# Kernel optimization log

Measured on AMD Instinct MI355X. Metric: run time of the kernel, lower is better.

The kernel has to match this reference:

```python
import jax, jax.numpy as jnp
import numpy as np

MAX_SEQ = 2048
NUM_HEADS = 32
NUM_KV_HEADS = 4
HEAD_DIM = 256
HIDDEN = 4096
ROTARY_DIM = 64  # head_dim * partial_rotary_factor(0.25)
THETA = 10000000.0
EPS = 1e-6
GROUPS = NUM_HEADS // NUM_KV_HEADS
SCALE = 1.0 / np.sqrt(HEAD_DIM)


def rms_norm(x, w):
    xf = x.astype(jnp.float32)
    norm = jax.lax.rsqrt(jnp.mean(xf * xf, axis=-1, keepdims=True) + EPS)
    return (xf * norm * w).astype(x.dtype)


def partial_rope(x, position):
    # x: [B, H, 1, D]; rotate first ROTARY_DIM dims (split-half convention)
    half = ROTARY_DIM // 2
    inv_freq = 1.0 / (THETA ** (jnp.arange(half, dtype=jnp.float32) / half))
    freqs = position.astype(jnp.float32) * inv_freq  # [half]
    cos = jnp.cos(freqs).reshape(1, 1, 1, -1)
    sin = jnp.sin(freqs).reshape(1, 1, 1, -1)
    x1 = x[..., :half]
    x2 = x[..., half:ROTARY_DIM]
    x_pass = x[..., ROTARY_DIM:]
    rot = jnp.concatenate([x1 * cos - x2 * sin, x2 * cos + x1 * sin], axis=-1)
    return jnp.concatenate([rot, x_pass], axis=-1)


def setup_inputs() -> dict:
    key = jax.random.key(0)
    ks = jax.random.split(key, 10)
    pos = 1500
    position = jnp.array([pos], dtype=jnp.int32)
    idx = jnp.arange(MAX_SEQ)
    mask = jnp.where(idx <= pos, 0.0, -1e9).astype(jnp.float32).reshape(1, 1, 1, MAX_SEQ)
    onehot = (idx == pos).astype(jnp.float32).reshape(1, 1, MAX_SEQ, 1)
    return {
        "x": jax.random.normal(ks[0], (1, 1, HIDDEN), dtype=jnp.float32),
        "position": position,
        "mask": mask,
        "k_cache": jax.random.normal(ks[1], (1, NUM_KV_HEADS, MAX_SEQ, HEAD_DIM), dtype=jnp.float32),
        "v_cache": jax.random.normal(ks[2], (1, NUM_KV_HEADS, MAX_SEQ, HEAD_DIM), dtype=jnp.float32),
        "onehot": onehot,
        "q_proj_w": jax.random.normal(ks[3], (2 * NUM_HEADS * HEAD_DIM, HIDDEN), dtype=jnp.float32) * 0.02,
        "k_proj_w": jax.random.normal(ks[4], (NUM_KV_HEADS * HEAD_DIM, HIDDEN), dtype=jnp.float32) * 0.02,
        "v_proj_w": jax.random.normal(ks[5], (NUM_KV_HEADS * HEAD_DIM, HIDDEN), dtype=jnp.float32) * 0.02,
        "o_proj_w": jax.random.normal(ks[6], (HIDDEN, NUM_HEADS * HEAD_DIM), dtype=jnp.float32) * 0.02,
        "q_norm_w": jnp.ones((HEAD_DIM,), dtype=jnp.float32),
        "k_norm_w": jnp.ones((HEAD_DIM,), dtype=jnp.float32),
    }


def reference(x, position, mask, k_cache, v_cache, onehot,
              q_proj_w, k_proj_w, v_proj_w, o_proj_w, q_norm_w, k_norm_w):
    B, T, _ = x.shape  # B=T=1
    # Q + gate interleaved per head
    qg = jnp.einsum('bth,oh->bto', x, q_proj_w).reshape(B, T, NUM_HEADS, 2 * HEAD_DIM)
    q = qg[..., :HEAD_DIM]                      # [B,T,H,D]
    gate = qg[..., HEAD_DIM:].reshape(B, T, -1)  # [B,T,H*D]
    q = jnp.transpose(q, (0, 2, 1, 3))           # [B,H,T,D]
    k = jnp.einsum('bth,oh->bto', x, k_proj_w).reshape(B, T, NUM_KV_HEADS, HEAD_DIM).transpose(0, 2, 1, 3)
    v = jnp.einsum('bth,oh->bto', x, v_proj_w).reshape(B, T, NUM_KV_HEADS, HEAD_DIM).transpose(0, 2, 1, 3)
    q = rms_norm(q, q_norm_w)
    k = rms_norm(k, k_norm_w)
    q = partial_rope(q, position)
    k = partial_rope(k, position)
    # full-buffer onehot cache update (same math as mul_/add_)
    k_cache = k_cache * (1.0 - onehot) + k * onehot  # [B,KV,S,D]
    v_cache = v_cache * (1.0 - onehot) + v * onehot
    # GQA: group query heads over kv heads without materializing expanded KV
    qg_heads = q.reshape(B, NUM_KV_HEADS, GROUPS, T, HEAD_DIM)
    attn = jnp.einsum('bgktd,bgsd->bgkts', qg_heads, k_cache) * SCALE  # [B,KV,G,T,S]
    attn = attn + mask[:, :, None]  # mask [B,1,1,T,S] broadcast
    attn = jax.nn.softmax(attn, axis=-1)
    out = jnp.einsum('bgkts,bgsd->bgktd', attn, v_cache)  # [B,KV,G,T,D]
    out = out.reshape(B, NUM_HEADS, T, HEAD_DIM).transpose(0, 2, 1, 3).reshape(B, T, -1)
    out = out * jax.nn.sigmoid(gate)
    return jnp.einsum('bto,ho->bth', out, o_proj_w)
```

## Files before the change

### kernel.cpp

```cpp
#include <hip/hip_runtime.h>
#include <math.h>

#define MAX_SEQ   2048
#define NUM_HEADS 32
#define NUM_KV    4
#define HEAD_DIM  256
#define HIDDEN    4096
#define ROT_DIM   64
#define GROUPS    8
#define SCALE     0.0625f
#define CHUNK     32
#define NCHUNK    (MAX_SEQ / CHUNK)

typedef float f4 __attribute__((ext_vector_type(4)));

__device__ inline f4 ntload4(const float* p) {
    return __builtin_nontemporal_load(reinterpret_cast<const f4*>(p));
}

__global__ void rope_table(const int* __restrict__ posp, float* __restrict__ tab) {
    const int i = threadIdx.x;
    if (i < 32) {
        const double inv_freq = pow(10000000.0, -(double)i / 32.0);
        const double ang = (double)posp[0] * inv_freq;
        tab[i]      = (float)cos(ang);
        tab[i + 32] = (float)sin(ang);
    }
}

__global__ __launch_bounds__(256) void gemv_qkv(
    const float* __restrict__ x,
    const float* __restrict__ qw,
    const float* __restrict__ kw,
    const float* __restrict__ vw,
    float* __restrict__ out)
{
    const int wave = threadIdx.x >> 6;
    const int lane = threadIdx.x & 63;
    const int row  = blockIdx.x * 4 + wave;

    const float* w;
    if (row < 16384)      w = qw + (size_t)row * HIDDEN;
    else if (row < 17408) w = kw + (size_t)(row - 16384) * HIDDEN;
    else                  w = vw + (size_t)(row - 17408) * HIDDEN;

    float acc = 0.f;
#pragma unroll
    for (int it = 0; it < HIDDEN / 256; ++it) {
        const int idx = it * 256 + lane * 4;
        f4 wv = ntload4(w + idx);
        f4 xv = *reinterpret_cast<const f4*>(x + idx);
        acc += wv[0] * xv[0] + wv[1] * xv[1] + wv[2] * xv[2] + wv[3] * xv[3];
    }
#pragma unroll
    for (int off = 32; off >= 1; off >>= 1) acc += __shfl_xor(acc, off);
    if (lane == 0) out[row] = acc;
}

__global__ __launch_bounds__(256) void attn_partial(
    const float* __restrict__ qkv,
    const float* __restrict__ qnw,
    const float* __restrict__ knw,
    const float* __restrict__ kcache,
    const float* __restrict__ vcache,
    const float* __restrict__ tab,
    const int*   __restrict__ posp,
    float* __restrict__ part_m,
    float* __restrict__ part_l,
    float* __restrict__ part_acc)
{
    const int kv  = blockIdx.x;
    const int c   = blockIdx.y;
    const int pos = posp[0];
    const int s0  = c * CHUNK;
    const int tid = threadIdx.x;

    if (s0 > pos) {
        if (tid == 0) {
#pragma unroll
            for (int g = 0; g < GROUPS; ++g) {
                const int pid = (kv * GROUPS + g) * NCHUNK + c;
                part_m[pid] = -1e30f; part_l[pid] = 0.f;
            }
        }
        return;
    }
    const int s1 = min(s0 + CHUNK, pos + 1);

    const int lane = tid & 63;
    const int wave = tid >> 6;
    const int d    = tid;

    float vals[9];
#pragma unroll
    for (int g = 0; g < GROUPS; ++g)
        vals[g] = qkv[(kv * GROUPS + g) * 512 + d];
    vals[8] = qkv[16384 + kv * HEAD_DIM + d];

    __shared__ float ssred[9][4];
    {
        float sq[9];
#pragma unroll
        for (int g = 0; g < 9; ++g) sq[g] = vals[g] * vals[g];
#pragma unroll
        for (int off = 32; off >= 1; off >>= 1) {
#pragma unroll
            for (int g = 0; g < 9; ++g) sq[g] += __shfl_xor(sq[g], off);
        }
        if (lane == 0) {
#pragma unroll
            for (int g = 0; g < 9; ++g) ssred[g][wave] = sq[g];
        }
    }
    __syncthreads();

    __shared__ __align__(16) float qn[9][HEAD_DIM];
    {
        const float qw_ = qnw[d];
        const float kw_ = knw[d];
#pragma unroll
        for (int g = 0; g < 9; ++g) {
            const float tot  = ssred[g][0] + ssred[g][1] + ssred[g][2] + ssred[g][3];
            const float norm = rsqrtf(tot * (1.0f / HEAD_DIM) + 1e-6f);
            qn[g][d] = vals[g] * norm * (g < 8 ? qw_ : kw_);
        }
    }
    __syncthreads();

    {
        const bool rot = (d < ROT_DIM);
        const int  i   = d & 31;
        const float co = tab[i];
        const float si = tab[i + 32];
        float rv[9];
#pragma unroll
        for (int g = 0; g < 9; ++g) {
            const float x1 = qn[g][i];
            const float x2 = qn[g][i + 32];
            rv[g] = (d < 32) ? (x1 * co - x2 * si) : (x2 * co + x1 * si);
        }
        __syncthreads();
        if (rot) {
#pragma unroll
            for (int g = 0; g < 9; ++g) qn[g][d] = rv[g];
        }
        __syncthreads();
    }

    const float* kbase = kcache + (size_t)kv * MAX_SEQ * HEAD_DIM;
    const float* vbase = vcache + (size_t)kv * MAX_SEQ * HEAD_DIM;

    f4 q8[GROUPS];
#pragma unroll
    for (int g = 0; g < GROUPS; ++g)
        q8[g] = *reinterpret_cast<const f4*>(&qn[g][lane * 4]);

    __shared__ float sc[GROUPS][CHUNK];
    __shared__ __align__(16) float pl[GROUPS][CHUNK];
    __shared__ float mh[GROUPS], lh[GROUPS];

    {
        const int i0 = wave * 8;
        f4 kvec[8];
#pragma unroll
        for (int j = 0; j < 8; ++j) {
            const int s = s0 + i0 + j;
            if (s < pos) kvec[j] = ntload4(kbase + (size_t)s * HEAD_DIM + lane * 4);
            else         kvec[j] = *reinterpret_cast<const f4*>(&qn[8][lane * 4]);
        }
#pragma unroll
        for (int j = 0; j < 8; ++j) {
            const int s = s0 + i0 + j;
            const bool valid = (s < s1);
            float part[GROUPS];
#pragma unroll
            for (int g = 0; g < GROUPS; ++g) {
                f4 t = q8[g] * kvec[j];
                part[g] = t[0] + t[1] + t[2] + t[3];
            }
#pragma unroll
            for (int off = 32; off >= 1; off >>= 1) {
#pragma unroll
                for (int g = 0; g < GROUPS; ++g)
                    part[g] += __shfl_xor(part[g], off);
            }
            if (lane == 0) {
#pragma unroll
                for (int g = 0; g < GROUPS; ++g)
                    sc[g][i0 + j] = valid ? part[g] * SCALE : -1e30f;
            }
        }
    }
    __syncthreads();

    {
        const int h = tid >> 5;
        const int j = tid & 31;
        float v = sc[h][j];
        float m = v;
#pragma unroll
        for (int off = 16; off >= 1; off >>= 1)
            m = fmaxf(m, __shfl_xor(m, off));
        const float p = expf(v - m);
        pl[h][j] = p;
        float ls = p;
#pragma unroll
        for (int off = 16; off >= 1; off >>= 1)
            ls += __shfl_xor(ls, off);
        if (j == 0) { mh[h] = m; lh[h] = ls; }
    }
    __syncthreads();

    float acc[GROUPS];
#pragma unroll
    for (int g = 0; g < GROUPS; ++g) acc[g] = 0.f;
    const float* vnew = qkv + 17408 + kv * HEAD_DIM;
#pragma unroll
    for (int i4 = 0; i4 < CHUNK / 4; ++i4) {
        float vv[4];
#pragma unroll
        for (int u = 0; u < 4; ++u) {
            const int s = s0 + i4 * 4 + u;
            vv[u] = (s < pos) ? __builtin_nontemporal_load(vbase + (size_t)s * HEAD_DIM + d)
                              : vnew[d];
        }
        f4 p4[GROUPS];
#pragma unroll
        for (int g = 0; g < GROUPS; ++g)
            p4[g] = *reinterpret_cast<const f4*>(&pl[g][i4 * 4]);
#pragma unroll
        for (int u = 0; u < 4; ++u) {
#pragma unroll
            for (int g = 0; g < GROUPS; ++g)
                acc[g] += p4[g][u] * vv[u];
        }
    }
#pragma unroll
    for (int g = 0; g < GROUPS; ++g) {
        const int pid = (kv * GROUPS + g) * NCHUNK + c;
        part_acc[(size_t)pid * HEAD_DIM + d] = acc[g];
        if (tid == 0) { part_m[pid] = mh[g]; part_l[pid] = lh[g]; }
    }
}

__global__ __launch_bounds__(256) void attn_combine(
    const float* __restrict__ part_m,
    const float* __restrict__ part_l,
    const float* __restrict__ part_acc,
    const float* __restrict__ qkv,
    float* __restrict__ attn_gated)
{
    const int h = blockIdx.x;
    const int d = threadIdx.x;

    float M = -1e30f;
    for (int c = 0; c < NCHUNK; ++c) M = fmaxf(M, part_m[h * NCHUNK + c]);

    float L = 0.f, acc = 0.f;
    for (int c = 0; c < NCHUNK; ++c) {
        const float lc = part_l[h * NCHUNK + c];
        if (lc > 0.f) {
            const float w = expf(part_m[h * NCHUNK + c] - M);
            L   += lc * w;
            acc += part_acc[(size_t)(h * NCHUNK + c) * HEAD_DIM + d] * w;
        }
    }
    const float o   = acc / L;
    const float g   = qkv[h * 512 + 256 + d];
    const float sig = 1.0f / (1.0f + expf(-g));
    attn_gated[h * HEAD_DIM + d] = o * sig;
}

__global__ __launch_bounds__(256) void gemv_o(
    const float* __restrict__ vec,
    const float* __restrict__ w,
    float* __restrict__ out)
{
    const int wave = threadIdx.x >> 6;
    const int lane = threadIdx.x & 63;
    const int row  = blockIdx.x * 4 + wave;
    const float* wr = w + (size_t)row * 8192;

    float acc = 0.f;
#pragma unroll
    for (int it = 0; it < 8192 / 256; ++it) {
        const int idx = it * 256 + lane * 4;
        f4 wv = ntload4(wr + idx);
        f4 xv = *reinterpret_cast<const f4*>(vec + idx);
        acc += wv[0] * xv[0] + wv[1] * xv[1] + wv[2] * xv[2] + wv[3] * xv[3];
    }
#pragma unroll
    for (int off = 32; off >= 1; off >>= 1) acc += __shfl_xor(acc, off);
    if (lane == 0) out[row] = acc;
}

extern "C" void kernel_launch(void* const* d_in, const int* in_sizes, int n_in,
                              void* d_out, int out_size, void* d_ws, size_t ws_size,
                              hipStream_t stream) {
    const float* x        = (const float*)d_in[0];
    const int*   position = (const int*)  d_in[1];
    const float* k_cache  = (const float*)d_in[3];
    const float* v_cache  = (const float*)d_in[4];
    const float* q_proj_w = (const float*)d_in[6];
    const float* k_proj_w = (const float*)d_in[7];
    const float* v_proj_w = (const float*)d_in[8];
    const float* o_proj_w = (const float*)d_in[9];
    const float* q_norm_w = (const float*)d_in[10];
    const float* k_norm_w = (const float*)d_in[11];
    float* out = (float*)d_out;

    float* ws         = (float*)d_ws;
    float* qkv        = ws;
    float* tab        = ws + 18432;
    float* part_m     = ws + 18496;
    float* part_l     = ws + 20544;
    float* part_acc   = ws + 22592;
    float* attn_gated = ws + 546880;

    rope_table<<<1, 64, 0, stream>>>(position, tab);
    gemv_qkv<<<18432 / 4, 256, 0, stream>>>(x, q_proj_w, k_proj_w, v_proj_w, qkv);
    dim3 g2(NUM_KV, NCHUNK);
    attn_partial<<<g2, 256, 0, stream>>>(qkv, q_norm_w, k_norm_w,
                                         k_cache, v_cache, tab, position,
                                         part_m, part_l, part_acc);
    attn_combine<<<NUM_HEADS, 256, 0, stream>>>(part_m, part_l, part_acc, qkv,
                                                attn_gated);
    gemv_o<<<4096 / 4, 256, 0, stream>>>(attn_gated, o_proj_w, out);
}
```

Before: 108.0 us.

## Fold rope table into QKV GEMV, two rows per wave, prefetch KV earlier, smaller chunks

The separate rope_table launch is folded into an extra block of the QKV GEMV. Both GEMVs now compute two output rows per wave and set launch_bounds occupancy hints. Attention partials use 16-position chunks, doubling the number of blocks, and issue the K and V cache loads before the RMS-norm and RoPE stage so their latency overlaps that work. The cost is more partial results for attn_combine to merge, higher register pressure from the prefetched values, and a reshuffled workspace layout.

```diff
diff --git a/kernel.cpp b/kernel.cpp
--- a/kernel.cpp
+++ b/kernel.cpp
@@ -9,7 +9,7 @@
 #define ROT_DIM   64
 #define GROUPS    8
 #define SCALE     0.0625f
-#define CHUNK     32
+#define CHUNK     16
 #define NCHUNK    (MAX_SEQ / CHUNK)
 
 typedef float f4 __attribute__((ext_vector_type(4)));
@@ -18,43 +18,54 @@
     return __builtin_nontemporal_load(reinterpret_cast<const f4*>(p));
 }
 
-__global__ void rope_table(const int* __restrict__ posp, float* __restrict__ tab) {
-    const int i = threadIdx.x;
-    if (i < 32) {
-        const double inv_freq = pow(10000000.0, -(double)i / 32.0);
-        const double ang = (double)posp[0] * inv_freq;
-        tab[i]      = (float)cos(ang);
-        tab[i + 32] = (float)sin(ang);
-    }
-}
-
-__global__ __launch_bounds__(256) void gemv_qkv(
+__global__ __launch_bounds__(256, 4) void gemv_qkv(
     const float* __restrict__ x,
     const float* __restrict__ qw,
     const float* __restrict__ kw,
     const float* __restrict__ vw,
-    float* __restrict__ out)
+    const int*   __restrict__ posp,
+    float* __restrict__ out,
+    float* __restrict__ tab)
 {
+    if (blockIdx.x == 2304) {
+        const int i = threadIdx.x;
+        if (i < 32) {
+            const double inv_freq = pow(10000000.0, -(double)i / 32.0);
+            const double ang = (double)posp[0] * inv_freq;
+            tab[i]      = (float)cos(ang);
+            tab[i + 32] = (float)sin(ang);
+        }
+        return;
+    }
     const int wave = threadIdx.x >> 6;
     const int lane = threadIdx.x & 63;
-    const int row  = blockIdx.x * 4 + wave;
-
-    const float* w;
-    if (row < 16384)      w = qw + (size_t)row * HIDDEN;
-    else if (row < 17408) w = kw + (size_t)(row - 16384) * HIDDEN;
-    else                  w = vw + (size_t)(row - 17408) * HIDDEN;
-
-    float acc = 0.f;
+    const int wid  = blockIdx.x * 4 + wave;
+    const int r0   = wid * 2;
+    const int r1   = r0 + 1;
+
+    const float* w0 = (r0 < 16384) ? qw + (size_t)r0 * HIDDEN
+                    : (r0 < 17408) ? kw + (size_t)(r0 - 16384) * HIDDEN
+                                   : vw + (size_t)(r0 - 17408) * HIDDEN;
+    const float* w1 = (r1 < 16384) ? qw + (size_t)r1 * HIDDEN
+                    : (r1 < 17408) ? kw + (size_t)(r1 - 16384) * HIDDEN
+                                   : vw + (size_t)(r1 - 17408) * HIDDEN;
+
+    float a0 = 0.f, a1 = 0.f;
 #pragma unroll
     for (int it = 0; it < HIDDEN / 256; ++it) {
         const int idx = it * 256 + lane * 4;
-        f4 wv = ntload4(w + idx);
-        f4 xv = *reinterpret_cast<const f4*>(x + idx);
-        acc += wv[0] * xv[0] + wv[1] * xv[1] + wv[2] * xv[2] + wv[3] * xv[3];
-    }
-#pragma unroll
-    for (int off = 32; off >= 1; off >>= 1) acc += __shfl_xor(acc, off);
-    if (lane == 0) out[row] = acc;
+        f4 xv  = *reinterpret_cast<const f4*>(x + idx);
+        f4 wv0 = ntload4(w0 + idx);
+        f4 wv1 = ntload4(w1 + idx);
+        a0 += wv0[0]*xv[0] + wv0[1]*xv[1] + wv0[2]*xv[2] + wv0[3]*xv[3];
+        a1 += wv1[0]*xv[0] + wv1[1]*xv[1] + wv1[2]*xv[2] + wv1[3]*xv[3];
+    }
+#pragma unroll
+    for (int off = 32; off >= 1; off >>= 1) {
+        a0 += __shfl_xor(a0, off);
+        a1 += __shfl_xor(a1, off);
+    }
+    if (lane == 0) { out[r0] = a0; out[r1] = a1; }
 }
 
 __global__ __launch_bounds__(256) void attn_partial(
@@ -96,6 +107,27 @@
     for (int g = 0; g < GROUPS; ++g)
         vals[g] = qkv[(kv * GROUPS + g) * 512 + d];
     vals[8] = qkv[16384 + kv * HEAD_DIM + d];
+    const float vnew_d = qkv[17408 + kv * HEAD_DIM + d];
+
+    const float* kbase = kcache + (size_t)kv * MAX_SEQ * HEAD_DIM;
+    const float* vbase = vcache + (size_t)kv * MAX_SEQ * HEAD_DIM;
+
+    float vpre[CHUNK];
+#pragma unroll
+    for (int u = 0; u < CHUNK; ++u) {
+        const int s = s0 + u;
+        const int srow = (s < pos) ? s : 0;
+        vpre[u] = __builtin_nontemporal_load(vbase + (size_t)srow * HEAD_DIM + d);
+    }
+
+    const int i0 = wave * 4;
+    f4 kpre[4];
+#pragma unroll
+    for (int j = 0; j < 4; ++j) {
+        const int s = s0 + i0 + j;
+        const int srow = (s < pos) ? s : 0;
+        kpre[j] = ntload4(kbase + (size_t)srow * HEAD_DIM + lane * 4);
+    }
 
     __shared__ float ssred[9][4];
     {
@@ -147,8 +179,13 @@
         __syncthreads();
     }
 
-    const float* kbase = kcache + (size_t)kv * MAX_SEQ * HEAD_DIM;
-    const float* vbase = vcache + (size_t)kv * MAX_SEQ * HEAD_DIM;
+#pragma unroll
+    for (int u = 0; u < CHUNK; ++u)
+        if (s0 + u >= pos) vpre[u] = vnew_d;
+    const f4 kf4 = *reinterpret_cast<const f4*>(&qn[8][lane * 4]);
+#pragma unroll
+    for (int j = 0; j < 4; ++j)
+        if (s0 + i0 + j >= pos) kpre[j] = kf4;
 
     f4 q8[GROUPS];
 #pragma unroll
@@ -159,53 +196,43 @@
     __shared__ __align__(16) float pl[GROUPS][CHUNK];
     __shared__ float mh[GROUPS], lh[GROUPS];
 
-    {
-        const int i0 = wave * 8;
-        f4 kvec[8];
-#pragma unroll
-        for (int j = 0; j < 8; ++j) {
-            const int s = s0 + i0 + j;
-            if (s < pos) kvec[j] = ntload4(kbase + (size_t)s * HEAD_DIM + lane * 4);
-            else         kvec[j] = *reinterpret_cast<const f4*>(&qn[8][lane * 4]);
-        }
-#pragma unroll
-        for (int j = 0; j < 8; ++j) {
-            const int s = s0 + i0 + j;
-            const bool valid = (s < s1);
-            float part[GROUPS];
-#pragma unroll
-            for (int g = 0; g < GROUPS; ++g) {
-                f4 t = q8[g] * kvec[j];
-                part[g] = t[0] + t[1] + t[2] + t[3];
-            }
-#pragma unroll
-            for (int off = 32; off >= 1; off >>= 1) {
-#pragma unroll
-                for (int g = 0; g < GROUPS; ++g)
-                    part[g] += __shfl_xor(part[g], off);
-            }
-            if (lane == 0) {
-#pragma unroll
-                for (int g = 0; g < GROUPS; ++g)
-                    sc[g][i0 + j] = valid ? part[g] * SCALE : -1e30f;
-            }
+#pragma unroll
+    for (int j = 0; j < 4; ++j) {
+        const int s = s0 + i0 + j;
+        const bool valid = (s < s1);
+        float part[GROUPS];
+#pragma unroll
+        for (int g = 0; g < GROUPS; ++g) {
+            f4 t = q8[g] * kpre[j];
+            part[g] = t[0] + t[1] + t[2] + t[3];
+        }
+#pragma unroll
+        for (int off = 32; off >= 1; off >>= 1) {
+#pragma unroll
+            for (int g = 0; g < GROUPS; ++g)
+                part[g] += __shfl_xor(part[g], off);
+        }
+        if (lane == 0) {
+#pragma unroll
+            for (int g = 0; g < GROUPS; ++g)
+                sc[g][i0 + j] = valid ? part[g] * SCALE : -1e30f;
         }
     }
     __syncthreads();
 
-    {
-        const int h = tid >> 5;
-        const int j = tid & 31;
+    if (tid < 128) {
+        const int h = tid >> 4;
+        const int j = tid & 15;
         float v = sc[h][j];
         float m = v;
 #pragma unroll
-        for (int off = 16; off >= 1; off >>= 1)
+        for (int off = 8; off >= 1; off >>= 1)
             m = fmaxf(m, __shfl_xor(m, off));
         const float p = expf(v - m);
         pl[h][j] = p;
         float ls = p;
 #pragma unroll
-        for (int off = 16; off >= 1; off >>= 1)
+        for (int off = 8; off >= 1; off >>= 1)
             ls += __shfl_xor(ls, off);
         if (j == 0) { mh[h] = m; lh[h] = ls; }
     }
@@ -214,16 +241,8 @@
     float acc[GROUPS];
 #pragma unroll
     for (int g = 0; g < GROUPS; ++g) acc[g] = 0.f;
-    const float* vnew = qkv + 17408 + kv * HEAD_DIM;
 #pragma unroll
     for (int i4 = 0; i4 < CHUNK / 4; ++i4) {
-        float vv[4];
-#pragma unroll
-        for (int u = 0; u < 4; ++u) {
-            const int s = s0 + i4 * 4 + u;
-            vv[u] = (s < pos) ? __builtin_nontemporal_load(vbase + (size_t)s * HEAD_DIM + d)
-                              : vnew[d];
-        }
         f4 p4[GROUPS];
 #pragma unroll
         for (int g = 0; g < GROUPS; ++g)
@@ -232,7 +251,7 @@
         for (int u = 0; u < 4; ++u) {
 #pragma unroll
             for (int g = 0; g < GROUPS; ++g)
-                acc[g] += p4[g][u] * vv[u];
+                acc[g] += p4[g][u] * vpre[i4 * 4 + u];
         }
     }
 #pragma unroll
@@ -254,9 +273,11 @@
     const int d = threadIdx.x;
 
     float M = -1e30f;
+#pragma unroll 8
     for (int c = 0; c < NCHUNK; ++c) M = fmaxf(M, part_m[h * NCHUNK + c]);
 
     float L = 0.f, acc = 0.f;
+#pragma unroll 4
     for (int c = 0; c < NCHUNK; ++c) {
         const float lc = part_l[h * NCHUNK + c];
         if (lc > 0.f) {
@@ -271,27 +292,34 @@
     attn_gated[h * HEAD_DIM + d] = o * sig;
 }
 
-__global__ __launch_bounds__(256) void gemv_o(
+__global__ __launch_bounds__(256, 4) void gemv_o(
     const float* __restrict__ vec,
     const float* __restrict__ w,
     float* __restrict__ out)
 {
     const int wave = threadIdx.x >> 6;
     const int lane = threadIdx.x & 63;
-    const int row  = blockIdx.x * 4 + wave;
-    const float* wr = w + (size_t)row * 8192;
-
-    float acc = 0.f;
+    const int wid  = blockIdx.x * 4 + wave;
+    const int r0   = wid * 2;
+    const float* w0 = w + (size_t)r0 * 8192;
+    const float* w1 = w0 + 8192;
+
+    float a0 = 0.f, a1 = 0.f;
 #pragma unroll
     for (int it = 0; it < 8192 / 256; ++it) {
         const int idx = it * 256 + lane * 4;
-        f4 wv = ntload4(wr + idx);
-        f4 xv = *reinterpret_cast<const f4*>(vec + idx);
-        acc += wv[0] * xv[0] + wv[1] * xv[1] + wv[2] * xv[2] + wv[3] * xv[3];
-    }
-#pragma unroll
-    for (int off = 32; off >= 1; off >>= 1) acc += __shfl_xor(acc, off);
-    if (lane == 0) out[row] = acc;
+        f4 xv  = *reinterpret_cast<const f4*>(vec + idx);
+        f4 wv0 = ntload4(w0 + idx);
+        f4 wv1 = ntload4(w1 + idx);
+        a0 += wv0[0]*xv[0] + wv0[1]*xv[1] + wv0[2]*xv[2] + wv0[3]*xv[3];
+        a1 += wv1[0]*xv[0] + wv1[1]*xv[1] + wv1[2]*xv[2] + wv1[3]*xv[3];
+    }
+#pragma unroll
+    for (int off = 32; off >= 1; off >>= 1) {
+        a0 += __shfl_xor(a0, off);
+        a1 += __shfl_xor(a1, off);
+    }
+    if (lane == 0) { out[r0] = a0; out[r0 + 1] = a1; }
 }
 
 extern "C" void kernel_launch(void* const* d_in, const int* in_sizes, int n_in,
@@ -313,17 +341,17 @@
     float* qkv        = ws;
     float* tab        = ws + 18432;
     float* part_m     = ws + 18496;
-    float* part_l     = ws + 20544;
-    float* part_acc   = ws + 22592;
-    float* attn_gated = ws + 546880;
-
-    rope_table<<<1, 64, 0, stream>>>(position, tab);
-    gemv_qkv<<<18432 / 4, 256, 0, stream>>>(x, q_proj_w, k_proj_w, v_proj_w, qkv);
+    float* part_l     = ws + 22592;
+    float* part_acc   = ws + 26688;
+    float* attn_gated = ws + 1075264;
+
+    gemv_qkv<<<2305, 256, 0, stream>>>(x, q_proj_w, k_proj_w, v_proj_w,
+                                       position, qkv, tab);
     dim3 g2(NUM_KV, NCHUNK);
     attn_partial<<<g2, 256, 0, stream>>>(qkv, q_norm_w, k_norm_w,
                                          k_cache, v_cache, tab, position,
                                          part_m, part_l, part_acc);
     attn_combine<<<NUM_HEADS, 256, 0, stream>>>(part_m, part_l, part_acc, qkv,
                                                 attn_gated);
-    gemv_o<<<4096 / 4, 256, 0, stream>>>(attn_gated, o_proj_w, out);
-}
+    gemv_o<<<512, 256, 0, stream>>>(attn_gated, o_proj_w, out);
+}
```

After: 126.6 us. 17.3% more time.
